# Kernel optimization log

Measured on AMD Instinct MI355X. Metric: run time of the kernel, lower is better.

Reference implementation:

```python
import jax, jax.numpy as jnp
import numpy as np

N = 50000   # nodes
E = 400000  # edges
R = 35      # num_relations
B = 12      # num_bases
C = 128     # hidden_conv_dim (heads=1)
T = 4       # node types: load, gen, load_gen, ext
HL = 38     # hidden_lin_dim
OUT = 2


def setup_inputs() -> dict:
    key = jax.random.key(0)
    ks = jax.random.split(key, 24)
    s = 0.1  # param scale
    inp = {
        'x': jax.random.normal(ks[0], (N, 2), jnp.float32),
        'edge_index': jax.random.randint(ks[1], (2, E), 0, N, jnp.int32),
        'edge_type': jax.random.randint(ks[2], (E,), 0, R, jnp.int32),
        'edge_attr': jax.random.normal(ks[3], (E, 2), jnp.float32),
        'node_type': jax.random.randint(ks[4], (N,), 0, T, jnp.int32),
        'basis': jax.random.normal(ks[5], (B, 2, C), jnp.float32) * s,
        'att_rel': jax.random.normal(ks[6], (R, B), jnp.float32) * s,
        'q_att': jax.random.normal(ks[7], (C, 1), jnp.float32) * s,
        'k_att': jax.random.normal(ks[8], (C, 1), jnp.float32) * s,
        'e_att': jax.random.normal(ks[9], (C, 1), jnp.float32) * s,
        'lin_edge_W': jax.random.normal(ks[10], (2, C), jnp.float32) * s,
        'conv_bias': jax.random.normal(ks[11], (C,), jnp.float32) * s,
        'lin0_W': jax.random.normal(ks[12], (T, C, HL), jnp.float32) * s,
        'lin0_b': jax.random.normal(ks[13], (T, HL), jnp.float32) * s,
        'lin1_W': jax.random.normal(ks[14], (T, HL, HL), jnp.float32) * s,
        'lin1_b': jax.random.normal(ks[15], (T, HL), jnp.float32) * s,
        'lin2_W': jax.random.normal(ks[16], (T, HL, HL), jnp.float32) * s,
        'lin2_b': jax.random.normal(ks[17], (T, HL), jnp.float32) * s,
        'fin_W': jax.random.normal(ks[18], (T, HL, OUT), jnp.float32) * s,
        'fin_b': jax.random.normal(ks[19], (T, OUT), jnp.float32) * s,
    }
    return inp


def _segment_softmax(alpha, dst, n):
    # PyG softmax: max is detached, eps=1e-16 on the denominator
    amax = jax.lax.stop_gradient(jax.ops.segment_max(alpha, dst, num_segments=n))
    ex = jnp.exp(alpha - amax[dst])
    den = jax.ops.segment_sum(ex, dst, num_segments=n) + 1e-16
    return ex / den[dst]


def _per_type_linear(xv, W, b, t):
    # apply node-type-specific Linear: [N,d] x [T,d,h] -> pick row type
    y = jnp.einsum('nd,tdh->nth', xv, W)              # [N,T,h]
    y = jnp.take_along_axis(y, t[:, None, None], axis=1)[:, 0]
    return y + b[t]


def reference(x, edge_index, edge_type, edge_attr, node_type,
              basis, att_rel, q_att, k_att, e_att, lin_edge_W, conv_bias,
              lin0_W, lin0_b, lin1_W, lin1_b, lin2_W, lin2_b, fin_W, fin_b):
    n = x.shape[0]
    src, dst = edge_index[0], edge_index[1]
    # RGATConv with basis decomposition: per-relation weight [R, in=2, C]
    w = jnp.einsum('rb,bio->rio', att_rel, basis)
    w_e = w[edge_type]                                 # [E,2,C] edge gather
    out_i = jnp.einsum('ei,eic->ec', x[dst], w_e)      # [E,C]
    out_j = jnp.einsum('ei,eic->ec', x[src], w_e)      # [E,C]
    ke = (edge_attr @ lin_edge_W) @ e_att              # [E,1]
    alpha = out_i @ q_att + out_j @ k_att + ke         # additive self-attention
    alpha = jax.nn.leaky_relu(alpha, 0.2)
    alpha = _segment_softmax(alpha, dst, n)            # across-relation segment softmax
    msg = alpha * out_j                                # heads=1 -> [E,C]
    agg = jax.ops.segment_sum(msg, dst, num_segments=n) + conv_bias
    h = jax.nn.leaky_relu(agg, 0.2)                    # forward activation (dropout: eval)
    t = node_type
    h = _per_type_linear(jax.nn.relu(h), lin0_W, lin0_b, t)
    h = _per_type_linear(jax.nn.relu(h), lin1_W, lin1_b, t)
    h = _per_type_linear(jax.nn.relu(h), lin2_W, lin2_b, t)
    out = _per_type_linear(h, fin_W, fin_b, t)         # [N,2]
    # load nodes (type 0): second output passes through abs
    load_out = jnp.concatenate([out[:, :1], jnp.abs(out[:, 1:2])], axis=1)
    return jnp.where((t == 0)[:, None], load_out, out)
```

## Files before the change

kernel.cpp:

```cpp
#include <hip/hip_runtime.h>
#include <math.h>

#define N_NODES 50000
#define N_EDGES 400000
#define R_REL   35
#define B_BASES 12
#define C_DIM   128
#define HL_DIM  38
#define RI2     70
#define NP      50304
#define NB_HIST 196
#define NBUCK   786
#define EPB     2048
#define CAP     704

#define OFF_WT     0
#define OFF_WQ     8960
#define OFF_WK     9030
#define OFF_LE     9100
#define OFF_META   9104
#define OFF_HBLK   9120
#define OFF_PERM   10688
#define OFF_INV    60688
#define OFF_ECUR   110992
#define OFF_EREC   123568
#define OFF_W0P    2336944
#define OFF_W1P    2357424
#define OFF_W2P    2363504

#define ST    0
#define HH    0
#define Y0T   0
#define Y1T   3264
#define Y2T   0
#define SM_DINV 8192
#define SM_FW   8256
#define SM_FB   8332
#define LDS_FLOATS 8334

__global__ __launch_bounds__(256) void k_init(const int* __restrict__ node_type,
                                              const float* __restrict__ basis,
                                              const float* __restrict__ att_rel,
                                              const float* __restrict__ q_att,
                                              const float* __restrict__ k_att,
                                              const float* __restrict__ e_att,
                                              const float* __restrict__ lin_edge_W,
                                              const float* __restrict__ lin0_W,
                                              const float* __restrict__ lin1_W,
                                              const float* __restrict__ lin2_W,
                                              float* __restrict__ ws) {
    int b = blockIdx.x, tid = threadIdx.x;
    if (b < NB_HIST) {
        __shared__ int lh[4];
        if (tid < 4) lh[tid] = 0;
        __syncthreads();
        int i = b * 256 + tid;
        if (i < N_NODES) atomicAdd(&lh[node_type[i]], 1);
        __syncthreads();
        if (tid < 4) ((int*)(ws + OFF_HBLK))[b * 4 + tid] = lh[tid];
    } else if (b < NB_HIST + 35) {
        int idx = (b - NB_HIST) * 256 + tid;
        if (idx < RI2 * C_DIM) {
            int c  = idx & (C_DIM - 1);
            int ri = idx >> 7;
            int r = ri >> 1, ii = ri & 1;
            float acc = 0.f;
            #pragma unroll
            for (int bb = 0; bb < B_BASES; ++bb)
                acc += att_rel[r * B_BASES + bb] * basis[(bb * 2 + ii) * C_DIM + c];
            ws[OFF_WT + idx] = acc;
        }
    } else if (b == NB_HIST + 35) {
        for (int i = tid; i < NBUCK * 16; i += 256) ((int*)(ws + OFF_ECUR))[i] = 0;
    } else if (b < NB_HIST + 36 + 36) {
        int lane = tid & 63, wv = tid >> 6;
        int u = (b - (NB_HIST + 36)) * 4 + wv;
        if (u < 2 * RI2) {
            int ri = (u < RI2) ? u : (u - RI2);
            int r = ri >> 1, ii = ri & 1;
            const float* av = att_rel + r * B_BASES;
            const float* bs = basis + ii * C_DIM;
            float w1 = 0.f, w2 = 0.f;
            #pragma unroll
            for (int bb = 0; bb < B_BASES; ++bb) {
                float a = av[bb];
                w1 += a * bs[bb * 2 * C_DIM + lane];
                w2 += a * bs[bb * 2 * C_DIM + 64 + lane];
            }
            const float* qk = (u < RI2) ? q_att : k_att;
            float s = w1 * qk[lane] + w2 * qk[64 + lane];
            #pragma unroll
            for (int off = 32; off; off >>= 1) s += __shfl_xor(s, off, 64);
            if (lane == 0) ws[((u < RI2) ? OFF_WQ : OFF_WK) + ri] = s;
        } else if (u < 2 * RI2 + 2) {
            int j = u - 2 * RI2;
            const float* er = lin_edge_W + j * C_DIM;
            float s = er[lane] * e_att[lane] + er[64 + lane] * e_att[64 + lane];
            #pragma unroll
            for (int off = 32; off; off >>= 1) s += __shfl_xor(s, off, 64);
            if (lane == 0) ws[OFF_LE + j] = s;
        }
    } else {
        int g = (b - (NB_HIST + 36 + 36)) * 256 + tid;
        for (int idx = g; idx < 4 * C_DIM * HL_DIM; idx += 16 * 256) {
            int tt = idx / (C_DIM * HL_DIM);
            int rem = idx - tt * (C_DIM * HL_DIM);
            int cc = rem / HL_DIM, j = rem - cc * HL_DIM;
            ws[OFF_W0P + tt * (C_DIM * 40) + cc * 40 + j] = lin0_W[idx];
        }
        for (int idx = g; idx < 4 * HL_DIM * HL_DIM; idx += 16 * 256) {
            int tt = idx / (HL_DIM * HL_DIM);
            int rem = idx - tt * (HL_DIM * HL_DIM);
            int cc = rem / HL_DIM, j = rem - cc * HL_DIM;
            ws[OFF_W1P + tt * (HL_DIM * 40) + cc * 40 + j] = lin1_W[idx];
            ws[OFF_W2P + tt * (HL_DIM * 40) + cc * 40 + j] = lin2_W[idx];
        }
    }
}

__global__ __launch_bounds__(256) void k_perm(const int* __restrict__ node_type,
                                              float* __restrict__ ws) {
    __shared__ int lh[NB_HIST * 4];
    __shared__ int pre[4], tot[4], basel[4];
    __shared__ int wcnt[4][4];
    int tid = threadIdx.x;
    int lane = tid & 63, wv = tid >> 6;
    const int* hblk = (const int*)(ws + OFF_HBLK);
    for (int i = tid; i < NB_HIST * 4; i += 256) lh[i] = hblk[i];
    __syncthreads();
    if (tid < 4) {
        int run = 0, mypre = 0;
        for (int bb = 0; bb < NB_HIST; ++bb) {
            if (bb == (int)blockIdx.x) mypre = run;
            run += lh[bb * 4 + tid];
        }
        pre[tid] = mypre;
        tot[tid] = run;
    }
    __syncthreads();
    if (tid == 0) {
        int t0 = tot[0], t1 = tot[1], t2 = tot[2];
        int b1 = ((t0 + 63) >> 6) << 6;
        int b2 = b1 + (((t1 + 63) >> 6) << 6);
        int b3 = b2 + (((t2 + 63) >> 6) << 6);
        basel[0] = 0; basel[1] = b1; basel[2] = b2; basel[3] = b3;
        if (blockIdx.x == 0) {
            int* meta = (int*)(ws + OFF_META);
            meta[0] = t0; meta[1] = t1; meta[2] = t2; meta[3] = tot[3];
            meta[4] = 0;  meta[5] = b1; meta[6] = b2; meta[7] = b3;
        }
    }
    __syncthreads();
    int n = blockIdx.x * 256 + tid;
    bool active = n < N_NODES;
    int ty = active ? node_type[n] : -1;
    int myrank = 0;
    #pragma unroll
    for (int t = 0; t < 4; ++t) {
        unsigned long long m = __ballot(ty == t);
        if (lane == 0) wcnt[wv][t] = __popcll(m);
        if (ty == t) myrank = __popcll(m & ((1ULL << lane) - 1ULL));
    }
    __syncthreads();
    if (active) {
        int prew = 0;
        for (int w2 = 0; w2 < wv; ++w2) prew += wcnt[w2][ty];
        int p = basel[ty] + pre[ty] + prew + myrank;
        ((int*)(ws + OFF_PERM))[n] = p;
        ((int*)(ws + OFF_INV))[p] = n;
    }
}

__global__ __launch_bounds__(256) void k_escatter(const float* __restrict__ x,
                                                  const int* __restrict__ edge_index,
                                                  const int* __restrict__ edge_type,
                                                  const float* __restrict__ edge_attr,
                                                  float* __restrict__ ws) {
    __shared__ int hist[NBUCK];
    __shared__ int sbase[NBUCK];
    __shared__ float swq[RI2], swk[RI2], sle[2];
    int tid = threadIdx.x;
    for (int i = tid; i < NBUCK; i += 256) hist[i] = 0;
    if (tid < RI2) { swq[tid] = ws[OFF_WQ + tid]; swk[tid] = ws[OFF_WK + tid]; }
    if (tid < 2) sle[tid] = ws[OFF_LE + tid];
    __syncthreads();

    const int* perm = (const int*)(ws + OFF_PERM);
    int base = blockIdx.x * EPB;
    int   rb[8], rm[8];
    float rex[8], rsx[8], rsy[8];
    #pragma unroll
    for (int k = 0; k < 8; ++k) {
        int e = base + k * 256 + tid;
        rb[k] = -1;
        if (e < N_EDGES) {
            int src = edge_index[e];
            int dst = edge_index[N_EDGES + e];
            int r   = edge_type[e];
            int p   = perm[dst];
            float2 ea = *(const float2*)(edge_attr + 2 * e);
            float2 xs = *(const float2*)(x + 2 * src);
            float2 xd = *(const float2*)(x + 2 * dst);
            float alpha = xd.x * swq[2 * r] + xd.y * swq[2 * r + 1]
                        + xs.x * swk[2 * r] + xs.y * swk[2 * r + 1]
                        + ea.x * sle[0]     + ea.y * sle[1];
            alpha = alpha > 0.f ? alpha : 0.2f * alpha;
            float ex = __expf(alpha);
            rb[k]  = p >> 6;
            rm[k]  = (r << 6) | (p & 63);
            rex[k] = ex;
            rsx[k] = ex * xs.x;
            rsy[k] = ex * xs.y;
            atomicAdd(&hist[rb[k]], 1);
        }
    }
    __syncthreads();
    int* gcur = (int*)(ws + OFF_ECUR);
    int rot = (blockIdx.x & 3) * 197;
    for (int i = tid; i < NBUCK; i += 256) {
        int j = i + rot; if (j >= NBUCK) j -= NBUCK;
        int c = hist[j];
        sbase[j] = (c > 0) ? atomicAdd(&gcur[j * 16], c) : 0;
    }
    __syncthreads();
    float4* rec = (float4*)(ws + OFF_EREC);
    #pragma unroll
    for (int k = 0; k < 8; ++k) {
        if (rb[k] >= 0) {
            int slot = atomicAdd(&sbase[rb[k]], 1);
            rec[(size_t)rb[k] * CAP + slot] =
                make_float4(__int_as_float(rm[k]), rex[k], rsx[k], rsy[k]);
        }
    }
}

__global__ __launch_bounds__(256, 4) void k_node(
        const float* __restrict__ ws, const float* __restrict__ conv_bias,
        const float* __restrict__ lin0_b, const float* __restrict__ lin1_b,
        const float* __restrict__ lin2_b, const float* __restrict__ fin_W,
        const float* __restrict__ fin_b, float* __restrict__ out) {
    __shared__ float L[LDS_FLOATS];
    int tid  = threadIdx.x;
    int lane = tid & 63;
    int wv   = tid >> 6;
    int p0   = blockIdx.x * 64;

    const int* meta = (const int*)(ws + OFF_META);
    int b1 = meta[5], b2 = meta[6], b3 = meta[7];
    int t  = (p0 >= b1) + (p0 >= b2) + (p0 >= b3);
    int bp = meta[4 + t];
    int cnt = meta[t];

    int ecnt = ((const int*)(ws + OFF_ECUR))[blockIdx.x * 16];
    const float4* rec = (const float4*)(ws + OFF_EREC) + (size_t)blockIdx.x * CAP;
    float4 rv0 = make_float4(0.f, 0.f, 0.f, 0.f), rv1 = rv0, rv2 = rv0;
    if (tid < ecnt)       rv0 = rec[tid];
    if (tid + 256 < ecnt) rv1 = rec[tid + 256];
    if (tid + 512 < ecnt) rv2 = rec[tid + 512];

    for (int i4 = tid; i4 < (RI2 * 68) / 4; i4 += 256)
        *(float4*)&L[ST + i4 * 4] = make_float4(0.f, 0.f, 0.f, 0.f);
    if (tid < 64) L[SM_DINV + tid] = 0.f;
    if (tid >= 64 && tid < 142) {
        int i = tid - 64;
        if (i < 76) L[SM_FW + i] = fin_W[t * 76 + i];
        else        L[SM_FB + i - 76] = fin_b[t * 2 + i - 76];
    }
    __syncthreads();

    if (tid < ecnt) {
        int m = __float_as_int(rv0.x);
        int n = m & 63, r = m >> 6;
        atomicAdd(&L[ST + (2 * r) * 68 + n],     rv0.z);
        atomicAdd(&L[ST + (2 * r + 1) * 68 + n], rv0.w);
        atomicAdd(&L[SM_DINV + n],               rv0.y);
    }
    if (tid + 256 < ecnt) {
        int m = __float_as_int(rv1.x);
        int n = m & 63, r = m >> 6;
        atomicAdd(&L[ST + (2 * r) * 68 + n],     rv1.z);
        atomicAdd(&L[ST + (2 * r + 1) * 68 + n], rv1.w);
        atomicAdd(&L[SM_DINV + n],               rv1.y);
    }
    if (tid + 512 < ecnt) {
        int m = __float_as_int(rv2.x);
        int n = m & 63, r = m >> 6;
        atomicAdd(&L[ST + (2 * r) * 68 + n],     rv2.z);
        atomicAdd(&L[ST + (2 * r + 1) * 68 + n], rv2.w);
        atomicAdd(&L[SM_DINV + n],               rv2.y);
    }
    __syncthreads();
    if (tid < 64) L[SM_DINV + tid] = 1.0f / (L[SM_DINV + tid] + 1e-16f);

    int ng = lane & 15, cg_ = lane >> 4;
    int c0 = wv * 32 + cg_ * 8;
    const float* wTg = ws + OFF_WT;
    float acc[32];
    #pragma unroll
    for (int i = 0; i < 32; ++i) acc[i] = 0.f;
    #pragma unroll 5
    for (int kk = 0; kk < RI2; ++kk) {
        float4 a4 = *(const float4*)&L[ST + kk * 68 + ng * 4];
        float4 wa = *(const float4*)&wTg[kk * 128 + c0];
        float4 wc = *(const float4*)&wTg[kk * 128 + c0 + 4];
        float a_[4] = {a4.x, a4.y, a4.z, a4.w};
        float w_[8] = {wa.x, wa.y, wa.z, wa.w, wc.x, wc.y, wc.z, wc.w};
        #pragma unroll
        for (int ni = 0; ni < 4; ++ni)
            #pragma unroll
            for (int ci = 0; ci < 8; ++ci)
                acc[ni * 8 + ci] += a_[ni] * w_[ci];
    }
    __syncthreads();

    {
        float4 dv = *(const float4*)&L[SM_DINV + ng * 4];
        float d_[4] = {dv.x, dv.y, dv.z, dv.w};
        #pragma unroll
        for (int ci = 0; ci < 8; ++ci) {
            float cb = conv_bias[c0 + ci];
            float4 hv;
            float h0 = acc[0 * 8 + ci] * d_[0] + cb;
            float h1 = acc[1 * 8 + ci] * d_[1] + cb;
            float h2 = acc[2 * 8 + ci] * d_[2] + cb;
            float h3 = acc[3 * 8 + ci] * d_[3] + cb;
            hv.x = h0 > 0.f ? h0 : 0.f;
            hv.y = h1 > 0.f ? h1 : 0.f;
            hv.z = h2 > 0.f ? h2 : 0.f;
            hv.w = h3 > 0.f ? h3 : 0.f;
            *(float4*)&L[HH + (c0 + ci) * 64 + ng * 4] = hv;
        }
    }
    __syncthreads();

    int jg = lane >> 4;
    int j0 = wv * 16 + jg * 4;
    const float* W0g = ws + OFF_W0P + t * (C_DIM * 40);
    float acc2[16];
    #pragma unroll
    for (int i = 0; i < 16; ++i) acc2[i] = 0.f;
    if (wv < 3) {
        #pragma unroll 4
        for (int kk = 0; kk < C_DIM; ++kk) {
            float4 a4 = *(const float4*)&L[HH + kk * 64 + ng * 4];
            float4 w4 = *(const float4*)&W0g[kk * 40 + j0];
            float a_[4] = {a4.x, a4.y, a4.z, a4.w};
            float w_[4] = {w4.x, w4.y, w4.z, w4.w};
            #pragma unroll
            for (int ni = 0; ni < 4; ++ni)
                #pragma unroll
                for (int ji = 0; ji < 4; ++ji)
                    acc2[ni * 4 + ji] += a_[ni] * w_[ji];
        }
    }
    __syncthreads();

    if (wv < 3) {
        #pragma unroll
        for (int ji = 0; ji < 4; ++ji) {
            int j = j0 + ji;
            float b = (j < HL_DIM) ? lin0_b[t * HL_DIM + j] : 0.f;
            float4 yv;
            float y0 = acc2[0 * 4 + ji] + b;
            float y1 = acc2[1 * 4 + ji] + b;
            float y2 = acc2[2 * 4 + ji] + b;
            float y3 = acc2[3 * 4 + ji] + b;
            yv.x = y0 > 0.f ? y0 : 0.f;
            yv.y = y1 > 0.f ? y1 : 0.f;
            yv.z = y2 > 0.f ? y2 : 0.f;
            yv.w = y3 > 0.f ? y3 : 0.f;
            *(float4*)&L[Y0T + j * 68 + ng * 4] = yv;
        }
    }
    __syncthreads();

    if (wv < 3) {
        const float* W1g = ws + OFF_W1P + t * (HL_DIM * 40);
        float acc3[16];
        #pragma unroll
        for (int i = 0; i < 16; ++i) acc3[i] = 0.f;
        #pragma unroll 2
        for (int kk = 0; kk < HL_DIM; ++kk) {
            float4 a4 = *(const float4*)&L[Y0T + kk * 68 + ng * 4];
            float4 w4 = *(const float4*)&W1g[kk * 40 + j0];
            float a_[4] = {a4.x, a4.y, a4.z, a4.w};
            float w_[4] = {w4.x, w4.y, w4.z, w4.w};
            #pragma unroll
            for (int ni = 0; ni < 4; ++ni)
                #pragma unroll
                for (int ji = 0; ji < 4; ++ji)
                    acc3[ni * 4 + ji] += a_[ni] * w_[ji];
        }
        #pragma unroll
        for (int ji = 0; ji < 4; ++ji) {
            int j = j0 + ji;
            float b = (j < HL_DIM) ? lin1_b[t * HL_DIM + j] : 0.f;
            float4 yv;
            float y0 = acc3[0 * 4 + ji] + b;
            float y1 = acc3[1 * 4 + ji] + b;
            float y2 = acc3[2 * 4 + ji] + b;
            float y3 = acc3[3 * 4 + ji] + b;
            yv.x = y0 > 0.f ? y0 : 0.f;
            yv.y = y1 > 0.f ? y1 : 0.f;
            yv.z = y2 > 0.f ? y2 : 0.f;
            yv.w = y3 > 0.f ? y3 : 0.f;
            *(float4*)&L[Y1T + j * 68 + ng * 4] = yv;
        }
    }
    __syncthreads();

    if (wv < 3) {
        const float* W2g = ws + OFF_W2P + t * (HL_DIM * 40);
        float acc4[16];
        #pragma unroll
        for (int i = 0; i < 16; ++i) acc4[i] = 0.f;
        #pragma unroll 2
        for (int kk = 0; kk < HL_DIM; ++kk) {
            float4 a4 = *(const float4*)&L[Y1T + kk * 68 + ng * 4];
            float4 w4 = *(const float4*)&W2g[kk * 40 + j0];
            float a_[4] = {a4.x, a4.y, a4.z, a4.w};
            float w_[4] = {w4.x, w4.y, w4.z, w4.w};
            #pragma unroll
            for (int ni = 0; ni < 4; ++ni)
                #pragma unroll
                for (int ji = 0; ji < 4; ++ji)
                    acc4[ni * 4 + ji] += a_[ni] * w_[ji];
        }
        #pragma unroll
        for (int ji = 0; ji < 4; ++ji) {
            int j = j0 + ji;
            float b = (j < HL_DIM) ? lin2_b[t * HL_DIM + j] : 0.f;
            float4 yv;
            yv.x = acc4[0 * 4 + ji] + b;
            yv.y = acc4[1 * 4 + ji] + b;
            yv.z = acc4[2 * 4 + ji] + b;
            yv.w = acc4[3 * 4 + ji] + b;
            *(float4*)&L[Y2T + j * 68 + ng * 4] = yv;
        }
    }
    __syncthreads();

    if (tid < 64) {
        int p = p0 + tid;
        bool valid = (p - bp) < cnt;
        float o0 = L[SM_FB], o1 = L[SM_FB + 1];
        for (int jj = 0; jj < HL_DIM; ++jj) {
            float v = L[Y2T + jj * 68 + tid];
            float2 f = *(const float2*)&L[SM_FW + jj * 2];
            o0 += v * f.x;
            o1 += v * f.y;
        }
        if (t == 0) o1 = fabsf(o1);
        if (valid) {
            int orig = ((const int*)(ws + OFF_INV))[p];
            ((float2*)out)[orig] = make_float2(o0, o1);
        }
    }
}

extern "C" void kernel_launch(void* const* d_in, const int* in_sizes, int n_in,
                              void* d_out, int out_size, void* d_ws, size_t ws_size,
                              hipStream_t stream) {
    const float* x          = (const float*)d_in[0];
    const int*   edge_index = (const int*)  d_in[1];
    const int*   edge_type  = (const int*)  d_in[2];
    const float* edge_attr  = (const float*)d_in[3];
    const int*   node_type  = (const int*)  d_in[4];
    const float* basis      = (const float*)d_in[5];
    const float* att_rel    = (const float*)d_in[6];
    const float* q_att      = (const float*)d_in[7];
    const float* k_att      = (const float*)d_in[8];
    const float* e_att      = (const float*)d_in[9];
    const float* lin_edge_W = (const float*)d_in[10];
    const float* conv_bias  = (const float*)d_in[11];
    const float* lin0_W     = (const float*)d_in[12];
    const float* lin0_b     = (const float*)d_in[13];
    const float* lin1_W     = (const float*)d_in[14];
    const float* lin1_b     = (const float*)d_in[15];
    const float* lin2_W     = (const float*)d_in[16];
    const float* lin2_b     = (const float*)d_in[17];
    const float* fin_W      = (const float*)d_in[18];
    const float* fin_b      = (const float*)d_in[19];

    float* ws  = (float*)d_ws;
    float* out = (float*)d_out;

    k_init    <<<NB_HIST + 35 + 1 + 36 + 16, 256, 0, stream>>>(node_type, basis, att_rel,
                                                               q_att, k_att, e_att, lin_edge_W,
                                                               lin0_W, lin1_W, lin2_W, ws);
    k_perm    <<<NB_HIST, 256, 0, stream>>>(node_type, ws);
    k_escatter<<<NB_HIST, 256, 0, stream>>>(x, edge_index, edge_type, edge_attr, ws);
    k_node    <<<NBUCK, 256, 0, stream>>>(ws, conv_bias,
                                          lin0_b, lin1_b, lin2_b, fin_W, fin_b, out);
}
```

Baseline: 172.6 us.

## Replace per-block type histogram and perm kernel with atomic rank assignment

Removes the separate k_perm kernel. k_init now assigns each node a rank within its type through wave-level ballots and global atomics, storing a packed (rank, type) word. k_escatter derives bucket positions from the type totals, and extra blocks in the same launch write the inverse permutation. A memset replaces the zeroing block. This saves one launch and its serial prefix pass, but node order inside each type now depends on atomic timing, which can change the reduction order.

```diff
diff --git a/kernel.cpp b/kernel.cpp
--- a/kernel.cpp
+++ b/kernel.cpp
@@ -19,14 +19,14 @@
 #define OFF_WK     9030
 #define OFF_LE     9100
 #define OFF_META   9104
-#define OFF_HBLK   9120
-#define OFF_PERM   10688
-#define OFF_INV    60688
-#define OFF_ECUR   110992
-#define OFF_EREC   123568
-#define OFF_W0P    2336944
-#define OFF_W1P    2357424
-#define OFF_W2P    2363504
+#define OFF_RTY    9120
+#define OFF_INV    59120
+#define OFF_TCNT   110976
+#define OFF_ECUR   111040
+#define OFF_EREC   123616
+#define OFF_W0P    2336992
+#define OFF_W1P    2357472
+#define OFF_W2P    2363552
 
 #define ST    0
 #define HH    0
@@ -50,35 +50,42 @@
                                               const float* __restrict__ lin2_W,
                                               float* __restrict__ ws) {
     int b = blockIdx.x, tid = threadIdx.x;
+    int lane = tid & 63, wv = tid >> 6;
     if (b < NB_HIST) {
-        __shared__ int lh[4];
-        if (tid < 4) lh[tid] = 0;
-        __syncthreads();
         int i = b * 256 + tid;
-        if (i < N_NODES) atomicAdd(&lh[node_type[i]], 1);
-        __syncthreads();
-        if (tid < 4) ((int*)(ws + OFF_HBLK))[b * 4 + tid] = lh[tid];
+        int ty = (i < N_NODES) ? node_type[i] : -1;
+        int* tcnt = (int*)(ws + OFF_TCNT);
+        int r = 0;
+        #pragma unroll
+        for (int t = 0; t < 4; ++t) {
+            unsigned long long m = __ballot(ty == t);
+            if (m) {
+                int leader = __ffsll((unsigned long long)m) - 1;
+                int base = 0;
+                if (lane == leader) base = atomicAdd(&tcnt[t * 16], __popcll(m));
+                base = __shfl(base, leader, 64);
+                if (ty == t) r = base + __popcll(m & ((1ULL << lane) - 1ULL));
+            }
+        }
+        if (i < N_NODES) ((int*)(ws + OFF_RTY))[i] = (r << 2) | ty;
     } else if (b < NB_HIST + 35) {
         int idx = (b - NB_HIST) * 256 + tid;
         if (idx < RI2 * C_DIM) {
             int c  = idx & (C_DIM - 1);
             int ri = idx >> 7;
-            int r = ri >> 1, ii = ri & 1;
+            int rr = ri >> 1, ii = ri & 1;
             float acc = 0.f;
             #pragma unroll
             for (int bb = 0; bb < B_BASES; ++bb)
-                acc += att_rel[r * B_BASES + bb] * basis[(bb * 2 + ii) * C_DIM + c];
+                acc += att_rel[rr * B_BASES + bb] * basis[(bb * 2 + ii) * C_DIM + c];
             ws[OFF_WT + idx] = acc;
         }
-    } else if (b == NB_HIST + 35) {
-        for (int i = tid; i < NBUCK * 16; i += 256) ((int*)(ws + OFF_ECUR))[i] = 0;
-    } else if (b < NB_HIST + 36 + 36) {
-        int lane = tid & 63, wv = tid >> 6;
-        int u = (b - (NB_HIST + 36)) * 4 + wv;
+    } else if (b < NB_HIST + 35 + 36) {
+        int u = (b - (NB_HIST + 35)) * 4 + wv;
         if (u < 2 * RI2) {
             int ri = (u < RI2) ? u : (u - RI2);
-            int r = ri >> 1, ii = ri & 1;
-            const float* av = att_rel + r * B_BASES;
+            int rr = ri >> 1, ii = ri & 1;
+            const float* av = att_rel + rr * B_BASES;
             const float* bs = basis + ii * C_DIM;
             float w1 = 0.f, w2 = 0.f;
             #pragma unroll
@@ -101,7 +108,7 @@
             if (lane == 0) ws[OFF_LE + j] = s;
         }
     } else {
-        int g = (b - (NB_HIST + 36 + 36)) * 256 + tid;
+        int g = (b - (NB_HIST + 35 + 36)) * 256 + tid;
         for (int idx = g; idx < 4 * C_DIM * HL_DIM; idx += 16 * 256) {
             int tt = idx / (C_DIM * HL_DIM);
             int rem = idx - tt * (C_DIM * HL_DIM);
@@ -118,75 +125,44 @@
     }
 }
 
-__global__ __launch_bounds__(256) void k_perm(const int* __restrict__ node_type,
-                                              float* __restrict__ ws) {
-    __shared__ int lh[NB_HIST * 4];
-    __shared__ int pre[4], tot[4], basel[4];
-    __shared__ int wcnt[4][4];
-    int tid = threadIdx.x;
-    int lane = tid & 63, wv = tid >> 6;
-    const int* hblk = (const int*)(ws + OFF_HBLK);
-    for (int i = tid; i < NB_HIST * 4; i += 256) lh[i] = hblk[i];
-    __syncthreads();
-    if (tid < 4) {
-        int run = 0, mypre = 0;
-        for (int bb = 0; bb < NB_HIST; ++bb) {
-            if (bb == (int)blockIdx.x) mypre = run;
-            run += lh[bb * 4 + tid];
-        }
-        pre[tid] = mypre;
-        tot[tid] = run;
-    }
-    __syncthreads();
-    if (tid == 0) {
-        int t0 = tot[0], t1 = tot[1], t2 = tot[2];
-        int b1 = ((t0 + 63) >> 6) << 6;
-        int b2 = b1 + (((t1 + 63) >> 6) << 6);
-        int b3 = b2 + (((t2 + 63) >> 6) << 6);
-        basel[0] = 0; basel[1] = b1; basel[2] = b2; basel[3] = b3;
-        if (blockIdx.x == 0) {
-            int* meta = (int*)(ws + OFF_META);
-            meta[0] = t0; meta[1] = t1; meta[2] = t2; meta[3] = tot[3];
-            meta[4] = 0;  meta[5] = b1; meta[6] = b2; meta[7] = b3;
-        }
-    }
-    __syncthreads();
-    int n = blockIdx.x * 256 + tid;
-    bool active = n < N_NODES;
-    int ty = active ? node_type[n] : -1;
-    int myrank = 0;
-    #pragma unroll
-    for (int t = 0; t < 4; ++t) {
-        unsigned long long m = __ballot(ty == t);
-        if (lane == 0) wcnt[wv][t] = __popcll(m);
-        if (ty == t) myrank = __popcll(m & ((1ULL << lane) - 1ULL));
-    }
-    __syncthreads();
-    if (active) {
-        int prew = 0;
-        for (int w2 = 0; w2 < wv; ++w2) prew += wcnt[w2][ty];
-        int p = basel[ty] + pre[ty] + prew + myrank;
-        ((int*)(ws + OFF_PERM))[n] = p;
-        ((int*)(ws + OFF_INV))[p] = n;
-    }
-}
-
 __global__ __launch_bounds__(256) void k_escatter(const float* __restrict__ x,
                                                   const int* __restrict__ edge_index,
                                                   const int* __restrict__ edge_type,
                                                   const float* __restrict__ edge_attr,
                                                   float* __restrict__ ws) {
+    int b = blockIdx.x, tid = threadIdx.x;
+    const int* tcnt = (const int*)(ws + OFF_TCNT);
+    int t0 = tcnt[0], t1 = tcnt[16], t2 = tcnt[32], t3 = tcnt[48];
+    int b1 = ((t0 + 63) >> 6) << 6;
+    int b2 = b1 + (((t1 + 63) >> 6) << 6);
+    int b3 = b2 + (((t2 + 63) >> 6) << 6);
+
+    if (b >= NB_HIST) {
+        if (b == NB_HIST && tid == 0) {
+            int* meta = (int*)(ws + OFF_META);
+            meta[0] = t0; meta[1] = t1; meta[2] = t2; meta[3] = t3;
+            meta[4] = 0;  meta[5] = b1; meta[6] = b2; meta[7] = b3;
+        }
+        int n = (b - NB_HIST) * 256 + tid;
+        if (n < N_NODES) {
+            int v = ((const int*)(ws + OFF_RTY))[n];
+            int ty = v & 3, r = v >> 2;
+            int bs = (ty == 0) ? 0 : ((ty == 1) ? b1 : ((ty == 2) ? b2 : b3));
+            ((int*)(ws + OFF_INV))[bs + r] = n;
+        }
+        return;
+    }
+
     __shared__ int hist[NBUCK];
     __shared__ int sbase[NBUCK];
     __shared__ float swq[RI2], swk[RI2], sle[2];
-    int tid = threadIdx.x;
     for (int i = tid; i < NBUCK; i += 256) hist[i] = 0;
     if (tid < RI2) { swq[tid] = ws[OFF_WQ + tid]; swk[tid] = ws[OFF_WK + tid]; }
     if (tid < 2) sle[tid] = ws[OFF_LE + tid];
     __syncthreads();
 
-    const int* perm = (const int*)(ws + OFF_PERM);
-    int base = blockIdx.x * EPB;
+    const int* rty = (const int*)(ws + OFF_RTY);
+    int base = b * EPB;
     int   rb[8], rm[8];
     float rex[8], rsx[8], rsy[8];
     #pragma unroll
@@ -196,18 +172,21 @@
         if (e < N_EDGES) {
             int src = edge_index[e];
             int dst = edge_index[N_EDGES + e];
-            int r   = edge_type[e];
-            int p   = perm[dst];
+            int rel = edge_type[e];
+            int v   = rty[dst];
+            int ty  = v & 3;
+            int bs  = (ty == 0) ? 0 : ((ty == 1) ? b1 : ((ty == 2) ? b2 : b3));
+            int p   = bs + (v >> 2);
             float2 ea = *(const float2*)(edge_attr + 2 * e);
             float2 xs = *(const float2*)(x + 2 * src);
             float2 xd = *(const float2*)(x + 2 * dst);
-            float alpha = xd.x * swq[2 * r] + xd.y * swq[2 * r + 1]
-                        + xs.x * swk[2 * r] + xs.y * swk[2 * r + 1]
-                        + ea.x * sle[0]     + ea.y * sle[1];
+            float alpha = xd.x * swq[2 * rel] + xd.y * swq[2 * rel + 1]
+                        + xs.x * swk[2 * rel] + xs.y * swk[2 * rel + 1]
+                        + ea.x * sle[0]       + ea.y * sle[1];
             alpha = alpha > 0.f ? alpha : 0.2f * alpha;
             float ex = __expf(alpha);
             rb[k]  = p >> 6;
-            rm[k]  = (r << 6) | (p & 63);
+            rm[k]  = (rel << 6) | (p & 63);
             rex[k] = ex;
             rsx[k] = ex * xs.x;
             rsy[k] = ex * xs.y;
@@ -216,7 +195,7 @@
     }
     __syncthreads();
     int* gcur = (int*)(ws + OFF_ECUR);
-    int rot = (blockIdx.x & 3) * 197;
+    int rot = (b & 3) * 197;
     for (int i = tid; i < NBUCK; i += 256) {
         int j = i + rot; if (j >= NBUCK) j -= NBUCK;
         int c = hist[j];
@@ -359,12 +338,12 @@
         #pragma unroll
         for (int ji = 0; ji < 4; ++ji) {
             int j = j0 + ji;
-            float b = (j < HL_DIM) ? lin0_b[t * HL_DIM + j] : 0.f;
+            float bb = (j < HL_DIM) ? lin0_b[t * HL_DIM + j] : 0.f;
             float4 yv;
-            float y0 = acc2[0 * 4 + ji] + b;
-            float y1 = acc2[1 * 4 + ji] + b;
-            float y2 = acc2[2 * 4 + ji] + b;
-            float y3 = acc2[3 * 4 + ji] + b;
+            float y0 = acc2[0 * 4 + ji] + bb;
+            float y1 = acc2[1 * 4 + ji] + bb;
+            float y2 = acc2[2 * 4 + ji] + bb;
+            float y3 = acc2[3 * 4 + ji] + bb;
             yv.x = y0 > 0.f ? y0 : 0.f;
             yv.y = y1 > 0.f ? y1 : 0.f;
             yv.z = y2 > 0.f ? y2 : 0.f;
@@ -394,12 +373,12 @@
         #pragma unroll
         for (int ji = 0; ji < 4; ++ji) {
             int j = j0 + ji;
-            float b = (j < HL_DIM) ? lin1_b[t * HL_DIM + j] : 0.f;
+            float bb = (j < HL_DIM) ? lin1_b[t * HL_DIM + j] : 0.f;
             float4 yv;
-            float y0 = acc3[0 * 4 + ji] + b;
-            float y1 = acc3[1 * 4 + ji] + b;
-            float y2 = acc3[2 * 4 + ji] + b;
-            float y3 = acc3[3 * 4 + ji] + b;
+            float y0 = acc3[0 * 4 + ji] + bb;
+            float y1 = acc3[1 * 4 + ji] + bb;
+            float y2 = acc3[2 * 4 + ji] + bb;
+            float y3 = acc3[3 * 4 + ji] + bb;
             yv.x = y0 > 0.f ? y0 : 0.f;
             yv.y = y1 > 0.f ? y1 : 0.f;
             yv.z = y2 > 0.f ? y2 : 0.f;
@@ -429,12 +408,12 @@
         #pragma unroll
         for (int ji = 0; ji < 4; ++ji) {
             int j = j0 + ji;
-            float b = (j < HL_DIM) ? lin2_b[t * HL_DIM + j] : 0.f;
+            float bb = (j < HL_DIM) ? lin2_b[t * HL_DIM + j] : 0.f;
             float4 yv;
-            yv.x = acc4[0 * 4 + ji] + b;
-            yv.y = acc4[1 * 4 + ji] + b;
-            yv.z = acc4[2 * 4 + ji] + b;
-            yv.w = acc4[3 * 4 + ji] + b;
+            yv.x = acc4[0 * 4 + ji] + bb;
+            yv.y = acc4[1 * 4 + ji] + bb;
+            yv.z = acc4[2 * 4 + ji] + bb;
+            yv.w = acc4[3 * 4 + ji] + bb;
             *(float4*)&L[Y2T + j * 68 + ng * 4] = yv;
         }
     }
@@ -485,11 +464,13 @@
     float* ws  = (float*)d_ws;
     float* out = (float*)d_out;
 
-    k_init    <<<NB_HIST + 35 + 1 + 36 + 16, 256, 0, stream>>>(node_type, basis, att_rel,
-                                                               q_att, k_att, e_att, lin_edge_W,
-                                                               lin0_W, lin1_W, lin2_W, ws);
-    k_perm    <<<NB_HIST, 256, 0, stream>>>(node_type, ws);
-    k_escatter<<<NB_HIST, 256, 0, stream>>>(x, edge_index, edge_type, edge_attr, ws);
+    hipMemsetAsync((char*)d_ws + (size_t)OFF_TCNT * 4, 0,
+                   (size_t)(OFF_EREC - OFF_TCNT) * 4, stream);
+
+    k_init    <<<NB_HIST + 35 + 36 + 16, 256, 0, stream>>>(node_type, basis, att_rel,
+                                                           q_att, k_att, e_att, lin_edge_W,
+                                                           lin0_W, lin1_W, lin2_W, ws);
+    k_escatter<<<NB_HIST * 2, 256, 0, stream>>>(x, edge_index, edge_type, edge_attr, ws);
     k_node    <<<NBUCK, 256, 0, stream>>>(ws, conv_bias,
                                           lin0_b, lin1_b, lin2_b, fin_W, fin_b, out);
 }
```

Result: slower. 193.9 us (+12.3%).
